# Kernel optimization log

Measured on AMD Instinct MI355X. Metric: run time of the kernel, lower is better.

## Reference

```python
import jax, jax.numpy as jnp
import numpy as np

B, T, D = 2, 4096, 2048
H, DH = 4, 32


def setup_inputs() -> dict:
    key = jax.random.key(0)
    k0, k1, k2, k3 = jax.random.split(key, 4)
    return {
        "hidden_states": jax.random.normal(k0, (B, T, D), dtype=jnp.float32),
        "Wq": jax.random.normal(k1, (H * DH, D), dtype=jnp.float32) * 0.02,
        "Ww": jax.random.normal(k2, (H, D), dtype=jnp.float32) * 0.02,
        "Wk": jax.random.normal(k3, (DH, D), dtype=jnp.float32) * 0.02,
    }


def reference(hidden_states, Wq, Ww, Wk):
    b, t, d = hidden_states.shape
    h, dh = Ww.shape[0], Wk.shape[0]
    # projections (nn.Linear: x @ W^T)
    q = (hidden_states @ Wq.T).reshape(b, t, h, dh)  # (B,T,H,Dh)
    w = hidden_states @ Ww.T                          # (B,T,H)
    k = hidden_states @ Wk.T                          # (B,T,Dh) shared across heads
    # multi-head QK^T -> ReLU -> per-head weighted sum (no softmax)
    raw = jnp.einsum('bthd,bsd->bths', q, k)          # (B,T,H,S)
    raw = jax.nn.relu(raw)
    index_scores = jnp.einsum('bths,bth->bts', raw, w)  # (B,T,S)
    return index_scores
```

## Files before the change

### kernel.cpp

```cpp
#include <hip/hip_runtime.h>
#include <hip/hip_bf16.h>

#define B_ 2
#define T_ 4096
#define D_ 2048
#define H_ 4
#define NC 176
#define ROWS (B_ * T_)
#define NT 11
#define TILE_E (16 * NC)
#define WTILE_E (16 * D_)

typedef __attribute__((ext_vector_type(8))) short short8;
typedef __attribute__((ext_vector_type(4))) short short4v;
typedef __attribute__((ext_vector_type(4))) float f32x4;
typedef __attribute__((ext_vector_type(4))) float float4v;

__device__ inline unsigned short f2bf(float f) {
  unsigned u = __float_as_uint(f);
  u += 0x7fffu + ((u >> 16) & 1u);
  return (unsigned short)(u >> 16);
}
__device__ inline float bf2f(unsigned short s) {
  return __uint_as_float(((unsigned)s) << 16);
}

__global__ __launch_bounds__(256) void pack_weights(const float* __restrict__ Wq,
                                                    const float* __restrict__ Ww,
                                                    const float* __restrict__ Wk,
                                                    unsigned short* __restrict__ Wcb) {
  int idx = blockIdx.x * 256 + threadIdx.x;
  if (idx >= NC * D_) return;
  int row = idx / D_, col = idx - row * D_;
  float v = 0.f;
  if (row < 128)       v = Wq[row * D_ + col];
  else if (row < 160)  v = Wk[(row - 128) * D_ + col];
  else if (row < 164)  v = Ww[(row - 160) * D_ + col];
  int n = row >> 4, r = row & 15;
  size_t dst = (size_t)n * WTILE_E + (size_t)(col >> 3) * 128 + r * 8 + (col & 7);
  Wcb[dst] = f2bf(v);
}

__global__ __launch_bounds__(256) void proj_kernel(const float* __restrict__ hs,
                                                   const unsigned short* __restrict__ Wcb,
                                                   unsigned short* __restrict__ Cb) {
  __shared__ f32x4 red[3][11][64];

  int wid  = threadIdx.x >> 6;
  int lane = threadIdx.x & 63;
  int lr = lane & 15, lo = lane >> 4;
  int row0 = blockIdx.x * 16;
  int k0   = wid * 512;

  const float*          ap    = hs  + (size_t)(row0 + lr) * D_ + k0 + lo * 8;
  const unsigned short* bbase = Wcb + (size_t)k0 * 16 + lo * 128 + lr * 8;

  f32x4 acc[11];
#pragma unroll
  for (int n = 0; n < 11; ++n) acc[n] = (f32x4){0.f, 0.f, 0.f, 0.f};

  float4v A0[2], A1[2];
  short8  Bv[2][11];

  A0[0] = *(const float4v*)(ap);
  A1[0] = *(const float4v*)(ap + 4);
#pragma unroll
  for (int n = 0; n < 11; ++n)
    Bv[0][n] = *(const short8*)(bbase + (size_t)n * WTILE_E);

#pragma unroll
  for (int s = 0; s < 16; ++s) {
    const int cur = s & 1, nxt = cur ^ 1;
    if (s < 15) {
      A0[nxt] = *(const float4v*)(ap + (s + 1) * 32);
      A1[nxt] = *(const float4v*)(ap + (s + 1) * 32 + 4);
#pragma unroll
      for (int n = 0; n < 11; ++n)
        Bv[nxt][n] = *(const short8*)(bbase + (size_t)n * WTILE_E + (s + 1) * 512);
    }
    short8 a;
#pragma unroll
    for (int i = 0; i < 4; ++i) {
      a[i]     = (short)f2bf(A0[cur][i]);
      a[i + 4] = (short)f2bf(A1[cur][i]);
    }
#pragma unroll
    for (int n = 0; n < 11; ++n)
      acc[n] = __builtin_amdgcn_mfma_f32_16x16x32_bf16(a, Bv[cur][n], acc[n], 0, 0, 0);
  }

  if (wid != 0) {
#pragma unroll
    for (int n = 0; n < 11; ++n) red[wid - 1][n][lane] = acc[n];
  }
  __syncthreads();

  if (wid == 0) {
#pragma unroll
    for (int n = 0; n < 11; ++n) {
      f32x4 r0 = red[0][n][lane], r1 = red[1][n][lane], r2 = red[2][n][lane];
#pragma unroll
      for (int r = 0; r < 4; ++r) acc[n][r] += r0[r] + r1[r] + r2[r];
    }
    unsigned short* cb = Cb + (size_t)(row0 >> 4) * TILE_E + (lr & 7);
#pragma unroll
    for (int n = 0; n < 11; ++n) {
      int oct = n * 2 + (lr >> 3);
#pragma unroll
      for (int r = 0; r < 4; ++r)
        cb[oct * 128 + (lo * 4 + r) * 8] = f2bf(acc[n][r]);
    }
  }
}

__global__ __launch_bounds__(256) void score_kernel(const unsigned short* __restrict__ Cb,
                                                    float* __restrict__ out) {
  int b = blockIdx.z, tb = blockIdx.y, sb = blockIdx.x;
  int wid  = threadIdx.x >> 6;
  int lane = threadIdx.x & 63;
  int lr = lane & 15, lo = lane >> 4;
  int wm = wid >> 1, wn = wid & 1;
  int t_base = tb * 128 + wm * 64;
  int s_base = sb * 128 + wn * 64;

  const unsigned short* C2 = Cb + (size_t)b * (T_ / 16) * TILE_E;
  float* O = out + (size_t)b * T_ * T_;

  short8 bf[4];
#pragma unroll
  for (int n = 0; n < 4; ++n)
    bf[n] = *(const short8*)(C2 + (size_t)((s_base >> 4) + n) * TILE_E +
                             (16 + lo) * 128 + lr * 8);

  const f32x4 zero = (f32x4){0.f, 0.f, 0.f, 0.f};

#pragma unroll
  for (int m = 0; m < 4; ++m) {
    const unsigned short* Ct = C2 + (size_t)((t_base >> 4) + m) * TILE_E;

    short8 af[H_];
#pragma unroll
    for (int h = 0; h < H_; ++h)
      af[h] = *(const short8*)(Ct + (h * 4 + lo) * 128 + lr * 8);

    float wv[4][H_];
    const unsigned short* wp = Ct + 20 * 128 + lo * 32;
#pragma unroll
    for (int r = 0; r < 4; ++r) {
      short4v w4 = *(const short4v*)(wp + r * 8);
#pragma unroll
      for (int h = 0; h < H_; ++h) wv[r][h] = bf2f((unsigned short)w4[h]);
    }

    int tc = t_base + m * 16 + lo * 4;
#pragma unroll
    for (int n = 0; n < 4; ++n) {
      f32x4 o = zero;
#pragma unroll
      for (int h = 0; h < H_; ++h) {
        f32x4 c = __builtin_amdgcn_mfma_f32_16x16x32_bf16(af[h], bf[n], zero, 0, 0, 0);
#pragma unroll
        for (int r = 0; r < 4; ++r) o[r] += wv[r][h] * fmaxf(c[r], 0.f);
      }
      int sc = s_base + n * 16 + lr;
#pragma unroll
      for (int r = 0; r < 4; ++r)
        O[(size_t)(tc + r) * T_ + sc] = o[r];
    }
  }
}

extern "C" void kernel_launch(void* const* d_in, const int* in_sizes, int n_in,
                              void* d_out, int out_size, void* d_ws, size_t ws_size,
                              hipStream_t stream) {
  const float* hs = (const float*)d_in[0];
  const float* Wq = (const float*)d_in[1];
  const float* Ww = (const float*)d_in[2];
  const float* Wk = (const float*)d_in[3];
  float* out = (float*)d_out;

  unsigned short* Wcb = (unsigned short*)d_ws;
  unsigned short* Cb  = (unsigned short*)((char*)d_ws + (1 << 20));

  pack_weights<<<(NC * D_ + 255) / 256, 256, 0, stream>>>(Wq, Ww, Wk, Wcb);
  proj_kernel<<<ROWS / 16, 256, 0, stream>>>(hs, Wcb, Cb);
  dim3 g(T_ / 128, T_ / 128, B_);
  score_kernel<<<g, 256, 0, stream>>>(Cb, out);
}
```

Before: 62.25 us.

## Process two row tiles per projection block and coalesce score stores via LDS

The projection kernel now computes 32 rows per block, so each loaded weight fragment feeds two MFMA tiles, halving weight traffic per row. The split-K reduction is reworked so all four waves write partials and two waves each reduce and store one tile. The score kernel stages each wave's 16x64 output tile in shared memory and writes it with 16-byte vector stores along rows instead of scattered 4-byte stores. The cost is more registers in the projection kernel, fewer blocks in flight, and extra LDS traffic in the score kernel.

```diff
diff --git a/kernel.cpp b/kernel.cpp
--- a/kernel.cpp
+++ b/kernel.cpp
@@ -7,7 +7,6 @@
 #define H_ 4
 #define NC 176
 #define ROWS (B_ * T_)
-#define NT 11
 #define TILE_E (16 * NC)
 #define WTILE_E (16 * D_)
 
@@ -44,26 +43,31 @@
 __global__ __launch_bounds__(256) void proj_kernel(const float* __restrict__ hs,
                                                    const unsigned short* __restrict__ Wcb,
                                                    unsigned short* __restrict__ Cb) {
-  __shared__ f32x4 red[3][11][64];
+  __shared__ f32x4 red[4][2][11][64];
 
   int wid  = threadIdx.x >> 6;
   int lane = threadIdx.x & 63;
   int lr = lane & 15, lo = lane >> 4;
-  int row0 = blockIdx.x * 16;
+  int row0 = blockIdx.x * 32;
   int k0   = wid * 512;
 
-  const float*          ap    = hs  + (size_t)(row0 + lr) * D_ + k0 + lo * 8;
+  const float* ap0 = hs + (size_t)(row0 + lr) * D_ + k0 + lo * 8;
+  const float* ap1 = ap0 + (size_t)16 * D_;
   const unsigned short* bbase = Wcb + (size_t)k0 * 16 + lo * 128 + lr * 8;
 
-  f32x4 acc[11];
-#pragma unroll
-  for (int n = 0; n < 11; ++n) acc[n] = (f32x4){0.f, 0.f, 0.f, 0.f};
-
-  float4v A0[2], A1[2];
+  f32x4 acc[2][11];
+#pragma unroll
+  for (int m = 0; m < 2; ++m)
+#pragma unroll
+    for (int n = 0; n < 11; ++n) acc[m][n] = (f32x4){0.f, 0.f, 0.f, 0.f};
+
+  float4v A[2][2][2];
   short8  Bv[2][11];
 
-  A0[0] = *(const float4v*)(ap);
-  A1[0] = *(const float4v*)(ap + 4);
+  A[0][0][0] = *(const float4v*)(ap0);
+  A[0][0][1] = *(const float4v*)(ap0 + 4);
+  A[1][0][0] = *(const float4v*)(ap1);
+  A[1][0][1] = *(const float4v*)(ap1 + 4);
 #pragma unroll
   for (int n = 0; n < 11; ++n)
     Bv[0][n] = *(const short8*)(bbase + (size_t)n * WTILE_E);
@@ -72,49 +76,59 @@
   for (int s = 0; s < 16; ++s) {
     const int cur = s & 1, nxt = cur ^ 1;
     if (s < 15) {
-      A0[nxt] = *(const float4v*)(ap + (s + 1) * 32);
-      A1[nxt] = *(const float4v*)(ap + (s + 1) * 32 + 4);
+      A[0][nxt][0] = *(const float4v*)(ap0 + (s + 1) * 32);
+      A[0][nxt][1] = *(const float4v*)(ap0 + (s + 1) * 32 + 4);
+      A[1][nxt][0] = *(const float4v*)(ap1 + (s + 1) * 32);
+      A[1][nxt][1] = *(const float4v*)(ap1 + (s + 1) * 32 + 4);
 #pragma unroll
       for (int n = 0; n < 11; ++n)
         Bv[nxt][n] = *(const short8*)(bbase + (size_t)n * WTILE_E + (s + 1) * 512);
     }
-    short8 a;
+    short8 a0, a1;
 #pragma unroll
     for (int i = 0; i < 4; ++i) {
-      a[i]     = (short)f2bf(A0[cur][i]);
-      a[i + 4] = (short)f2bf(A1[cur][i]);
-    }
-#pragma unroll
-    for (int n = 0; n < 11; ++n)
-      acc[n] = __builtin_amdgcn_mfma_f32_16x16x32_bf16(a, Bv[cur][n], acc[n], 0, 0, 0);
+      a0[i]     = (short)f2bf(A[0][cur][0][i]);
+      a0[i + 4] = (short)f2bf(A[0][cur][1][i]);
+      a1[i]     = (short)f2bf(A[1][cur][0][i]);
+      a1[i + 4] = (short)f2bf(A[1][cur][1][i]);
+    }
+#pragma unroll
+    for (int n = 0; n < 11; ++n) {
+      acc[0][n] = __builtin_amdgcn_mfma_f32_16x16x32_bf16(a0, Bv[cur][n], acc[0][n], 0, 0, 0);
+      acc[1][n] = __builtin_amdgcn_mfma_f32_16x16x32_bf16(a1, Bv[cur][n], acc[1][n], 0, 0, 0);
+    }
   }
 
-  if (wid != 0) {
-#pragma unroll
-    for (int n = 0; n < 11; ++n) red[wid - 1][n][lane] = acc[n];
-  }
+#pragma unroll
+  for (int m = 0; m < 2; ++m)
+#pragma unroll
+    for (int n = 0; n < 11; ++n) red[wid][m][n][lane] = acc[m][n];
   __syncthreads();
 
-  if (wid == 0) {
+  if (wid < 2) {
+    const int m = wid;
+    unsigned short* cb = Cb + (size_t)((row0 >> 4) + m) * TILE_E + (lr & 7);
 #pragma unroll
     for (int n = 0; n < 11; ++n) {
-      f32x4 r0 = red[0][n][lane], r1 = red[1][n][lane], r2 = red[2][n][lane];
-#pragma unroll
-      for (int r = 0; r < 4; ++r) acc[n][r] += r0[r] + r1[r] + r2[r];
-    }
-    unsigned short* cb = Cb + (size_t)(row0 >> 4) * TILE_E + (lr & 7);
-#pragma unroll
-    for (int n = 0; n < 11; ++n) {
+      f32x4 t = red[0][m][n][lane];
+#pragma unroll
+      for (int w = 1; w < 4; ++w) {
+        f32x4 p = red[w][m][n][lane];
+#pragma unroll
+        for (int r = 0; r < 4; ++r) t[r] += p[r];
+      }
       int oct = n * 2 + (lr >> 3);
 #pragma unroll
       for (int r = 0; r < 4; ++r)
-        cb[oct * 128 + (lo * 4 + r) * 8] = f2bf(acc[n][r]);
+        cb[oct * 128 + (lo * 4 + r) * 8] = f2bf(t[r]);
     }
   }
 }
 
 __global__ __launch_bounds__(256) void score_kernel(const unsigned short* __restrict__ Cb,
                                                     float* __restrict__ out) {
+  __shared__ __align__(16) float tbuf[4][16][72];
+
   int b = blockIdx.z, tb = blockIdx.y, sb = blockIdx.x;
   int wid  = threadIdx.x >> 6;
   int lane = threadIdx.x & 63;
@@ -133,6 +147,8 @@
                              (16 + lo) * 128 + lr * 8);
 
   const f32x4 zero = (f32x4){0.f, 0.f, 0.f, 0.f};
+  int rr = lane >> 4;
+  int cq = (lane & 15) * 4;
 
 #pragma unroll
   for (int m = 0; m < 4; ++m) {
@@ -152,7 +168,7 @@
       for (int h = 0; h < H_; ++h) wv[r][h] = bf2f((unsigned short)w4[h]);
     }
 
-    int tc = t_base + m * 16 + lo * 4;
+    f32x4 o4[4];
 #pragma unroll
     for (int n = 0; n < 4; ++n) {
       f32x4 o = zero;
@@ -162,10 +178,20 @@
 #pragma unroll
         for (int r = 0; r < 4; ++r) o[r] += wv[r][h] * fmaxf(c[r], 0.f);
       }
-      int sc = s_base + n * 16 + lr;
+      o4[n] = o;
+    }
+
+#pragma unroll
+    for (int n = 0; n < 4; ++n)
 #pragma unroll
       for (int r = 0; r < 4; ++r)
-        O[(size_t)(tc + r) * T_ + sc] = o[r];
+        tbuf[wid][lo * 4 + r][n * 16 + lr] = o4[n][r];
+
+    float* Om = O + (size_t)(t_base + m * 16) * T_ + s_base;
+#pragma unroll
+    for (int j = 0; j < 4; ++j) {
+      float4v v = *(const float4v*)&tbuf[wid][rr + 4 * j][cq];
+      *(float4v*)(Om + (size_t)(rr + 4 * j) * T_ + cq) = v;
     }
   }
 }
@@ -183,7 +209,7 @@
   unsigned short* Cb  = (unsigned short*)((char*)d_ws + (1 << 20));
 
   pack_weights<<<(NC * D_ + 255) / 256, 256, 0, stream>>>(Wq, Ww, Wk, Wcb);
-  proj_kernel<<<ROWS / 16, 256, 0, stream>>>(hs, Wcb, Cb);
+  proj_kernel<<<ROWS / 32, 256, 0, stream>>>(hs, Wcb, Cb);
   dim3 g(T_ / 128, T_ / 128, B_);
   score_kernel<<<g, 256, 0, stream>>>(Cb, out);
 }
```

Result: slower. 65.25 us (+4.8%).

## Deepen projection prefetch pipeline and stage score outputs through LDS for vector stores

Applied to the files above, without the earlier changes.

The projection kernel's register prefetch goes from double buffering to a three-deep pipeline for weights and four-deep for activations, to hide more global load latency. The score kernel now writes each 16x64 output tile into a per-wave shared-memory buffer and reads it back so every lane stores 16-byte float4 rows instead of scattered 4-byte stores. The output write is the dominant traffic, so wider, coalesced stores should cut store transactions. In exchange, register pressure in the projection kernel rises and the score kernel adds LDS use and round trips.

```diff
diff --git a/kernel.cpp b/kernel.cpp
--- a/kernel.cpp
+++ b/kernel.cpp
@@ -7,7 +7,6 @@
 #define H_ 4
 #define NC 176
 #define ROWS (B_ * T_)
-#define NT 11
 #define TILE_E (16 * NC)
 #define WTILE_E (16 * D_)
 
@@ -59,34 +58,40 @@
 #pragma unroll
   for (int n = 0; n < 11; ++n) acc[n] = (f32x4){0.f, 0.f, 0.f, 0.f};
 
-  float4v A0[2], A1[2];
-  short8  Bv[2][11];
-
-  A0[0] = *(const float4v*)(ap);
-  A1[0] = *(const float4v*)(ap + 4);
-#pragma unroll
-  for (int n = 0; n < 11; ++n)
-    Bv[0][n] = *(const short8*)(bbase + (size_t)n * WTILE_E);
+  float4v A0[4], A1[4];
+  short8  Bv[3][11];
+
+#pragma unroll
+  for (int p = 0; p < 3; ++p) {
+    A0[p] = *(const float4v*)(ap + p * 32);
+    A1[p] = *(const float4v*)(ap + p * 32 + 4);
+  }
+#pragma unroll
+  for (int p = 0; p < 2; ++p)
+#pragma unroll
+    for (int n = 0; n < 11; ++n)
+      Bv[p][n] = *(const short8*)(bbase + (size_t)n * WTILE_E + p * 512);
 
 #pragma unroll
   for (int s = 0; s < 16; ++s) {
-    const int cur = s & 1, nxt = cur ^ 1;
-    if (s < 15) {
-      A0[nxt] = *(const float4v*)(ap + (s + 1) * 32);
-      A1[nxt] = *(const float4v*)(ap + (s + 1) * 32 + 4);
+    if (s + 3 < 16) {
+      A0[(s + 3) & 3] = *(const float4v*)(ap + (s + 3) * 32);
+      A1[(s + 3) & 3] = *(const float4v*)(ap + (s + 3) * 32 + 4);
+    }
+    if (s + 2 < 16) {
 #pragma unroll
       for (int n = 0; n < 11; ++n)
-        Bv[nxt][n] = *(const short8*)(bbase + (size_t)n * WTILE_E + (s + 1) * 512);
+        Bv[(s + 2) % 3][n] = *(const short8*)(bbase + (size_t)n * WTILE_E + (s + 2) * 512);
     }
     short8 a;
 #pragma unroll
     for (int i = 0; i < 4; ++i) {
-      a[i]     = (short)f2bf(A0[cur][i]);
-      a[i + 4] = (short)f2bf(A1[cur][i]);
+      a[i]     = (short)f2bf(A0[s & 3][i]);
+      a[i + 4] = (short)f2bf(A1[s & 3][i]);
     }
 #pragma unroll
     for (int n = 0; n < 11; ++n)
-      acc[n] = __builtin_amdgcn_mfma_f32_16x16x32_bf16(a, Bv[cur][n], acc[n], 0, 0, 0);
+      acc[n] = __builtin_amdgcn_mfma_f32_16x16x32_bf16(a, Bv[s % 3][n], acc[n], 0, 0, 0);
   }
 
   if (wid != 0) {
@@ -115,6 +120,8 @@
 
 __global__ __launch_bounds__(256) void score_kernel(const unsigned short* __restrict__ Cb,
                                                     float* __restrict__ out) {
+  __shared__ __align__(16) float tbuf[4][16][72];
+
   int b = blockIdx.z, tb = blockIdx.y, sb = blockIdx.x;
   int wid  = threadIdx.x >> 6;
   int lane = threadIdx.x & 63;
@@ -133,6 +140,8 @@
                              (16 + lo) * 128 + lr * 8);
 
   const f32x4 zero = (f32x4){0.f, 0.f, 0.f, 0.f};
+  int rr = lane >> 4;
+  int cq = (lane & 15) * 4;
 
 #pragma unroll
   for (int m = 0; m < 4; ++m) {
@@ -152,7 +161,7 @@
       for (int h = 0; h < H_; ++h) wv[r][h] = bf2f((unsigned short)w4[h]);
     }
 
-    int tc = t_base + m * 16 + lo * 4;
+    f32x4 o4[4];
 #pragma unroll
     for (int n = 0; n < 4; ++n) {
       f32x4 o = zero;
@@ -162,10 +171,20 @@
 #pragma unroll
         for (int r = 0; r < 4; ++r) o[r] += wv[r][h] * fmaxf(c[r], 0.f);
       }
-      int sc = s_base + n * 16 + lr;
+      o4[n] = o;
+    }
+
+#pragma unroll
+    for (int n = 0; n < 4; ++n)
 #pragma unroll
       for (int r = 0; r < 4; ++r)
-        O[(size_t)(tc + r) * T_ + sc] = o[r];
+        tbuf[wid][lo * 4 + r][n * 16 + lr] = o4[n][r];
+
+    float* Om = O + (size_t)(t_base + m * 16) * T_ + s_base;
+#pragma unroll
+    for (int j = 0; j < 4; ++j) {
+      float4v v = *(const float4v*)&tbuf[wid][rr + 4 * j][cq];
+      *(float4v*)(Om + (size_t)(rr + 4 * j) * T_ + cq) = v;
     }
   }
 }
```

Result: no change. 62.55 us (+0.5%).
